# Kernel optimization log

Measured on AMD Instinct MI355X. Metric: run time of the kernel, lower is better.

Reference implementation:

```python
import jax, jax.numpy as jnp
import numpy as np

IN_FEATURES = 896
OUT_FEATURES = 151936  # Qwen2.5 vocab
BATCH, SEQ = 2, 1024


def setup_inputs() -> dict:
    key = jax.random.key(0)
    k1, k2, k3 = jax.random.split(key, 3)
    x = jax.random.normal(k1, (BATCH, SEQ, IN_FEATURES), dtype=jnp.float32)
    # int8-range quantized weights stored as int32 (values in [-127, 127])
    quant_weight = jax.random.randint(k2, (OUT_FEATURES, IN_FEATURES), -127, 128, dtype=jnp.int32)
    # per-output-row scales (positive, small)
    scales = jax.random.uniform(k3, (OUT_FEATURES,), dtype=jnp.float32, minval=0.001, maxval=0.02)
    return {"x": x, "quant_weight": quant_weight, "scales": scales}


def reference(x, quant_weight, scales):
    # dequantize: W = int8_weight * per_row_scale  -> [out, in]
    w = quant_weight.astype(x.dtype) * scales.astype(x.dtype)[:, None]
    # F.linear(x, W, None) == x @ W.T : [b, s, in] x [out, in] -> [b, s, out]
    return jnp.einsum('bsi,oi->bso', x, w)
```

## Files before the change

kernel.cpp:

```cpp
#include <hip/hip_runtime.h>
#include <hip/hip_bf16.h>


#define M_DIM 2048
#define N_DIM 151936
#define K_DIM 896

#define BM 128
#define BN 64
#define BK 64
#define NKT (K_DIM / BK)
#define MB_CNT (M_DIM / BM)
#define NB_CNT (N_DIM / BN)
#define NWG (MB_CNT * NB_CNT)

typedef __attribute__((ext_vector_type(8))) short bf16x8;
typedef __attribute__((ext_vector_type(4))) float f32x4;
typedef __attribute__((ext_vector_type(4))) int   i32x4;
typedef __attribute__((ext_vector_type(4))) unsigned int u32x4;
typedef __attribute__((ext_vector_type(2))) unsigned int u32x2;

static __device__ __forceinline__ unsigned short f2bf(float f) {
    unsigned int u = __builtin_bit_cast(unsigned int, f);
    u += 0x7FFFu + ((u >> 16) & 1u);
    return (unsigned short)(u >> 16);
}
static __device__ __forceinline__ unsigned int pack2(float lo, float hi) {
    return (unsigned int)f2bf(lo) | ((unsigned int)f2bf(hi) << 16);
}
static __device__ __forceinline__ void gload_lds16(const void* g, void* l) {
    __builtin_amdgcn_global_load_lds(
        (const __attribute__((address_space(1))) unsigned int*)g,
        (__attribute__((address_space(3))) unsigned int*)l, 16, 0, 0);
}


__global__ void quant_x_kernel(const float* __restrict__ X,
                               signed char* __restrict__ Xq,
                               float* __restrict__ Sx) {
    const int row  = blockIdx.x * 4 + (threadIdx.x >> 6);
    const int lane = threadIdx.x & 63;
    const float* xr = X + (size_t)row * K_DIM;
    float v[14];
    float am = 0.f;
    #pragma unroll
    for (int i = 0; i < 14; ++i) {
        v[i] = xr[lane + i * 64];
        am = fmaxf(am, fabsf(v[i]));
    }
    #pragma unroll
    for (int off = 32; off > 0; off >>= 1)
        am = fmaxf(am, __shfl_xor(am, off));
    am = fmaxf(am, 1e-20f);
    const float inv = 127.f / am;
    if (lane == 0) Sx[row] = am / 127.f;
    signed char* qr = Xq + (size_t)row * K_DIM;
    #pragma unroll
    for (int i = 0; i < 14; ++i)
        qr[lane + i * 64] = (signed char)(int)rintf(v[i] * inv);
}

__global__ void cvt_w8_kernel(const int* __restrict__ Wq,
                              signed char* __restrict__ W8) {
    const long n8 = (long)N_DIM * K_DIM / 8;
    for (long i = (long)blockIdx.x * blockDim.x + threadIdx.x; i < n8;
         i += (long)gridDim.x * blockDim.x) {
        i32x4 a = ((const i32x4*)Wq)[2 * i];
        i32x4 b = ((const i32x4*)Wq)[2 * i + 1];
        unsigned int lo = (unsigned int)(a[0] & 0xff) |
                          ((unsigned int)(a[1] & 0xff) << 8) |
                          ((unsigned int)(a[2] & 0xff) << 16) |
                          ((unsigned int)(a[3] & 0xff) << 24);
        unsigned int hi = (unsigned int)(b[0] & 0xff) |
                          ((unsigned int)(b[1] & 0xff) << 8) |
                          ((unsigned int)(b[2] & 0xff) << 16) |
                          ((unsigned int)(b[3] & 0xff) << 24);
        u32x2 o; o[0] = lo; o[1] = hi;
        ((u32x2*)W8)[i] = o;
    }
}


#define SCHED0 __builtin_amdgcn_sched_barrier(0)
#define VMCNT0 asm volatile("s_waitcnt vmcnt(0)" ::: "memory")
#define LGKM0  asm volatile("s_waitcnt lgkmcnt(0)" ::: "memory")

__global__ __launch_bounds__(256, 5)
void lmhead_gemm_i8(const signed char* __restrict__ Xq,
                    const signed char* __restrict__ W8,
                    const float* __restrict__ Sw,
                    const float* __restrict__ Sx,
                    float* __restrict__ O)
{
    __shared__ signed char ldsA[2][BM][BK];
    __shared__ signed char ldsB[2][BN][BK];

    const int tid  = threadIdx.x;
    const int lane = tid & 63;
    const int wave = tid >> 6;
    const int wr   = wave >> 1;
    const int wc   = wave & 1;

    const int bid = blockIdx.x;
    const int wg  = (bid & 7) * (NWG / 8) + (bid >> 3);
    const int mb  = wg % MB_CNT;
    const int nb  = wg / MB_CNT;

    const int lslot = (lane & 3) ^ ((lane >> 3) & 3);
    const signed char* srcA =
        Xq + (size_t)(mb * BM + wave * 32 + (lane >> 2)) * K_DIM + lslot * 16;
    const signed char* srcB =
        W8 + (size_t)(nb * BN + wave * 16 + (lane >> 2)) * K_DIM + lslot * 16;

    auto stage = [&](int b2, int k0) {
        gload_lds16(srcA + k0, &ldsA[b2][wave * 32][0]);
        gload_lds16(srcA + (size_t)16 * K_DIM + k0, &ldsA[b2][wave * 32 + 16][0]);
        gload_lds16(srcB + k0, &ldsB[b2][wave * 16][0]);
    };

    const int physoff   = ((lane >> 4) ^ ((lane >> 1) & 3)) * 16;
    const int arow_base = wr * 64 + (lane & 15);
    const int brow_base = wc * 32 + (lane & 15);

    i32x4 acc[4][2];
    #pragma unroll
    for (int i = 0; i < 4; ++i)
        #pragma unroll
        for (int j = 0; j < 2; ++j)
            acc[i][j] = i32x4{0, 0, 0, 0};

    stage(0, 0);
    SCHED0;
    VMCNT0;
    SCHED0;
    __builtin_amdgcn_s_barrier();
    SCHED0;

    i32x4 af[4], bfr[2];

#define READ_AB(B2) do { \
    _Pragma("unroll") \
    for (int mf = 0; mf < 4; ++mf) \
        af[mf] = *(const i32x4*)&ldsA[B2][arow_base + mf * 16][physoff]; \
    _Pragma("unroll") \
    for (int nf = 0; nf < 2; ++nf) \
        bfr[nf] = *(const i32x4*)&ldsB[B2][brow_base + nf * 16][physoff]; \
} while (0)
#define MFMA8() do { \
    __builtin_amdgcn_s_setprio(1); \
    _Pragma("unroll") \
    for (int mf = 0; mf < 4; ++mf) { \
        _Pragma("unroll") \
        for (int nf = 0; nf < 2; ++nf) \
            acc[mf][nf] = __builtin_amdgcn_mfma_i32_16x16x64_i8( \
                af[mf], bfr[nf], acc[mf][nf], 0, 0, 0); \
    } \
    __builtin_amdgcn_s_setprio(0); \
} while (0)

    #pragma unroll 2
    for (int t = 0; t < NKT; ++t) {
        const int cur = t & 1;
        READ_AB(cur);
        if (t < NKT - 1) stage(cur ^ 1, (t + 1) * BK);
        SCHED0;
        VMCNT0;
        LGKM0;
        SCHED0;
        __builtin_amdgcn_s_barrier();
        SCHED0;
        MFMA8();
    }

#undef READ_AB
#undef MFMA8

    __syncthreads();

    float* lf = (float*)&ldsA[0][0][0];
    const int qw = lane >> 4;
    const int li = lane & 15;

    float scn[2];
    #pragma unroll
    for (int nf = 0; nf < 2; ++nf)
        scn[nf] = Sw[nb * BN + wc * 32 + nf * 16 + li];

    #pragma unroll
    for (int p = 0; p < 2; ++p) {
        if (p) __syncthreads();
        if (wr == p) {
            #pragma unroll
            for (int a = 0; a < 4; ++a) {
                #pragma unroll
                for (int nf = 0; nf < 2; ++nf) {
                    #pragma unroll
                    for (int r = 0; r < 4; ++r) {
                        const int lr   = a * 16 + qw * 4 + r;
                        const int col  = wc * 32 + nf * 16 + li;
                        const int pcol = col ^ (qw << 4);
                        lf[lr * 64 + pcol] = (float)acc[a][nf][r] * scn[nf];
                    }
                }
            }
        }
        __syncthreads();
        #pragma unroll
        for (int i = 0; i < 4; ++i) {
            const int row    = i * 16 + (tid >> 4);
            const int lane16 = tid & 15;
            const int q      = (row >> 2) & 3;
            const int pch    = lane16 ^ (q << 2);
            f32x4 v = *(const f32x4*)&lf[row * 64 + pch * 4];
            const size_t grow = (size_t)(mb * BM + p * 64 + row);
            v *= Sx[grow];
            const size_t gcol = (size_t)(nb * BN + lane16 * 4);
            *(f32x4*)&O[grow * N_DIM + gcol] = v;
        }
    }
}


#define FBM 128
#define FBN 128
#define FBK 32
#define FNSTEPS (K_DIM / FBK)
#define FMB (M_DIM / FBM)
#define FNB (N_DIM / FBN)
#define FNWG (FMB * FNB)

__global__ __launch_bounds__(256, 2)
void lmhead_gemm_conv(const float* __restrict__ X,
                      const int* __restrict__ Wq,
                      const float* __restrict__ S,
                      float* __restrict__ O)
{
    __shared__ unsigned short Alds[2][FBM][FBK];
    __shared__ unsigned short Blds2[2][FBN][FBK];

    const int tid  = threadIdx.x;
    const int lane = tid & 63;
    const int wave = tid >> 6;
    const int wr   = wave >> 1;
    const int wc   = wave & 1;

    const int bid = blockIdx.x;
    const int wg  = (bid & 7) * (FNWG / 8) + (bid >> 3);
    const int mb  = wg % FMB;
    const int nb  = wg / FMB;

    const int srow = tid >> 1;
    const int skh  = (tid & 1) * 16;

    const float* aptr = X  + (size_t)(mb * FBM + srow) * K_DIM + skh;
    const int*   wptr = Wq + (size_t)(nb * FBN + srow) * K_DIM + skh;

    f32x4 av[4];
    i32x4 wv[4];

    auto load_tiles = [&](int k0) {
        const f32x4* ap = (const f32x4*)(aptr + k0);
        const i32x4* wp = (const i32x4*)(wptr + k0);
        av[0] = ap[0]; av[1] = ap[1]; av[2] = ap[2]; av[3] = ap[3];
        wv[0] = wp[0]; wv[1] = wp[1]; wv[2] = wp[2]; wv[3] = wp[3];
    };

    auto stage = [&](int buf) {
        unsigned int apk[8], wpk[8];
        #pragma unroll
        for (int i = 0; i < 8; ++i) {
            apk[i] = pack2(av[(2*i) >> 2][(2*i) & 3], av[(2*i+1) >> 2][(2*i+1) & 3]);
            wpk[i] = pack2((float)wv[(2*i) >> 2][(2*i) & 3], (float)wv[(2*i+1) >> 2][(2*i+1) & 3]);
        }
        *(u32x4*)&Alds[buf][srow][skh]      = u32x4{apk[0], apk[1], apk[2], apk[3]};
        *(u32x4*)&Alds[buf][srow][skh + 8]  = u32x4{apk[4], apk[5], apk[6], apk[7]};
        *(u32x4*)&Blds2[buf][srow][skh]     = u32x4{wpk[0], wpk[1], wpk[2], wpk[3]};
        *(u32x4*)&Blds2[buf][srow][skh + 8] = u32x4{wpk[4], wpk[5], wpk[6], wpk[7]};
    };

    f32x4 acc[4][4];
    #pragma unroll
    for (int i = 0; i < 4; ++i)
        #pragma unroll
        for (int j = 0; j < 4; ++j)
            acc[i][j] = f32x4{0.f, 0.f, 0.f, 0.f};

    load_tiles(0);
    stage(0);
    __syncthreads();

    int cur = 0;
    for (int s = 0; s < FNSTEPS; ++s) {
        if (s + 1 < FNSTEPS) load_tiles((s + 1) * FBK);

        bf16x8 af[4], bfr[4];
        const int arow = wr * 64 + (lane & 15);
        const int brow = wc * 64 + (lane & 15);
        const int kb   = (lane >> 4) * 8;
        #pragma unroll
        for (int mf = 0; mf < 4; ++mf)
            af[mf] = *(const bf16x8*)&Alds[cur][arow + mf * 16][kb];
        #pragma unroll
        for (int nf = 0; nf < 4; ++nf)
            bfr[nf] = *(const bf16x8*)&Blds2[cur][brow + nf * 16][kb];

        #pragma unroll
        for (int mf = 0; mf < 4; ++mf)
            #pragma unroll
            for (int nf = 0; nf < 4; ++nf)
                acc[mf][nf] = __builtin_amdgcn_mfma_f32_16x16x32_bf16(
                    af[mf], bfr[nf], acc[mf][nf], 0, 0, 0);

        if (s + 1 < FNSTEPS) stage(cur ^ 1);
        __syncthreads();
        cur ^= 1;
    }

    #pragma unroll
    for (int nf = 0; nf < 4; ++nf) {
        const int n = nb * FBN + wc * 64 + nf * 16 + (lane & 15);
        const float sc = S[n];
        #pragma unroll
        for (int mf = 0; mf < 4; ++mf) {
            const int m0 = mb * FBM + wr * 64 + mf * 16 + ((lane >> 4) << 2);
            #pragma unroll
            for (int r = 0; r < 4; ++r)
                O[(size_t)(m0 + r) * N_DIM + n] = acc[mf][nf][r] * sc;
        }
    }
}


extern "C" void kernel_launch(void* const* d_in, const int* in_sizes, int n_in,
                              void* d_out, int out_size, void* d_ws, size_t ws_size,
                              hipStream_t stream) {
    const float* X  = (const float*)d_in[0];
    const int*   Wq = (const int*)d_in[1];
    const float* S  = (const float*)d_in[2];
    float*       O  = (float*)d_out;

    const size_t XQ_BYTES = (size_t)M_DIM * K_DIM;
    const size_t SX_BYTES = (size_t)M_DIM * sizeof(float);
    const size_t W8_BYTES = (size_t)N_DIM * K_DIM;

    if (ws_size >= XQ_BYTES + SX_BYTES + W8_BYTES) {
        signed char* xq = (signed char*)d_ws;
        float*       sx = (float*)((char*)d_ws + XQ_BYTES);
        signed char* w8 = (signed char*)((char*)d_ws + XQ_BYTES + SX_BYTES);
        quant_x_kernel<<<M_DIM / 4, 256, 0, stream>>>(X, xq, sx);
        cvt_w8_kernel<<<2048, 256, 0, stream>>>(Wq, w8);
        lmhead_gemm_i8<<<NWG, 256, 0, stream>>>(xq, w8, S, sx, O);
    } else {
        lmhead_gemm_conv<<<FNWG, 256, 0, stream>>>(X, Wq, S, O);
    }
}
```

Before: 774.3 us.

## Keep full-K weight strip resident in LDS and stream activations from global

Each workgroup now loads a 128-column by full-K int8 weight strip into LDS once, using about 112 KB. It then loops over 1024 rows of M in chunks of 256, reading A fragments straight from global memory with even/odd register double-buffering. Blocks grow to 512 threads at one block per CU, and the double-buffered per-K-tile LDS staging and per-tile barriers are gone. The epilogue writes scaled results directly from registers instead of staging through LDS. That trades the earlier 16-byte vector stores for scalar stores covering 16 contiguous floats per row, which may hurt write coalescing on this output-heavy kernel.

```diff
diff --git a/kernel.cpp b/kernel.cpp
--- a/kernel.cpp
+++ b/kernel.cpp
@@ -6,13 +6,9 @@
 #define N_DIM 151936
 #define K_DIM 896
 
-#define BM 128
-#define BN 64
-#define BK 64
-#define NKT (K_DIM / BK)
-#define MB_CNT (M_DIM / BM)
-#define NB_CNT (N_DIM / BN)
-#define NWG (MB_CNT * NB_CNT)
+#define NKT 14
+#define NSTRIP (N_DIM / 128)
+#define NWG (NSTRIP * 2)
 
 typedef __attribute__((ext_vector_type(8))) short bf16x8;
 typedef __attribute__((ext_vector_type(4))) float f32x4;
@@ -81,141 +77,120 @@
 }
 
 
-#define SCHED0 __builtin_amdgcn_sched_barrier(0)
-#define VMCNT0 asm volatile("s_waitcnt vmcnt(0)" ::: "memory")
-#define LGKM0  asm volatile("s_waitcnt lgkmcnt(0)" ::: "memory")
-
-__global__ __launch_bounds__(256, 5)
+__global__ __launch_bounds__(512, 1)
 void lmhead_gemm_i8(const signed char* __restrict__ Xq,
                     const signed char* __restrict__ W8,
                     const float* __restrict__ Sw,
                     const float* __restrict__ Sx,
                     float* __restrict__ O)
 {
-    __shared__ signed char ldsA[2][BM][BK];
-    __shared__ signed char ldsB[2][BN][BK];
+    __shared__ signed char Wlds[NKT][128][64];
 
     const int tid  = threadIdx.x;
     const int lane = tid & 63;
     const int wave = tid >> 6;
-    const int wr   = wave >> 1;
+    const int mq   = wave >> 1;
     const int wc   = wave & 1;
 
     const int bid = blockIdx.x;
-    const int wg  = (bid & 7) * (NWG / 8) + (bid >> 3);
-    const int mb  = wg % MB_CNT;
-    const int nb  = wg / MB_CNT;
+    const int xcd = bid & 7, lin = bid >> 3;
+    const int q = NWG / 8, r = NWG % 8;
+    const int wg = (xcd < r ? xcd * (q + 1)
+                            : r * (q + 1) + (xcd - r) * q) + lin;
+    const int nb = wg >> 1;
+    const int mh = wg & 1;
 
     const int lslot = (lane & 3) ^ ((lane >> 3) & 3);
-    const signed char* srcA =
-        Xq + (size_t)(mb * BM + wave * 32 + (lane >> 2)) * K_DIM + lslot * 16;
-    const signed char* srcB =
-        W8 + (size_t)(nb * BN + wave * 16 + (lane >> 2)) * K_DIM + lslot * 16;
-
-    auto stage = [&](int b2, int k0) {
-        gload_lds16(srcA + k0, &ldsA[b2][wave * 32][0]);
-        gload_lds16(srcA + (size_t)16 * K_DIM + k0, &ldsA[b2][wave * 32 + 16][0]);
-        gload_lds16(srcB + k0, &ldsB[b2][wave * 16][0]);
-    };
-
-    const int physoff   = ((lane >> 4) ^ ((lane >> 1) & 3)) * 16;
-    const int arow_base = wr * 64 + (lane & 15);
-    const int brow_base = wc * 32 + (lane & 15);
-
-    i32x4 acc[4][2];
-    #pragma unroll
-    for (int i = 0; i < 4; ++i)
-        #pragma unroll
-        for (int j = 0; j < 2; ++j)
-            acc[i][j] = i32x4{0, 0, 0, 0};
-
-    stage(0, 0);
-    SCHED0;
-    VMCNT0;
-    SCHED0;
-    __builtin_amdgcn_s_barrier();
-    SCHED0;
-
-    i32x4 af[4], bfr[2];
-
-#define READ_AB(B2) do { \
+    const signed char* srcW =
+        W8 + (size_t)(nb * 128 + wave * 16 + (lane >> 2)) * K_DIM + lslot * 16;
+    #pragma unroll
+    for (int kt = 0; kt < NKT; ++kt)
+        gload_lds16(srcW + kt * 64, &Wlds[kt][wave * 16][0]);
+    asm volatile("s_waitcnt vmcnt(0)" ::: "memory");
+    __syncthreads();
+
+    const int physoff = ((lane >> 4) ^ ((lane >> 1) & 3)) * 16;
+    const int brow    = wc * 64 + (lane & 15);
+
+    float scn[4];
+    #pragma unroll
+    for (int nf = 0; nf < 4; ++nf)
+        scn[nf] = Sw[nb * 128 + wc * 64 + nf * 16 + (lane & 15)];
+
+    const int li  = lane & 15;
+    const int qw4 = (lane >> 4) * 4;
+
+    for (int s = 0; s < 4; ++s) {
+        const int mbase = mh * 1024 + s * 256;
+        const int mrow0 = mbase + mq * 64;
+
+        const signed char* aPtr =
+            Xq + (size_t)(mrow0 + li) * K_DIM + (lane >> 4) * 16;
+
+        f32x4 sxv0 = *(const f32x4*)&Sx[mrow0 +  0 + qw4];
+        f32x4 sxv1 = *(const f32x4*)&Sx[mrow0 + 16 + qw4];
+        f32x4 sxv2 = *(const f32x4*)&Sx[mrow0 + 32 + qw4];
+        f32x4 sxv3 = *(const f32x4*)&Sx[mrow0 + 48 + qw4];
+
+        i32x4 acc[4][4];
+        #pragma unroll
+        for (int i = 0; i < 4; ++i)
+            #pragma unroll
+            for (int j = 0; j < 4; ++j)
+                acc[i][j] = i32x4{0, 0, 0, 0};
+
+        i32x4 afE[4], afO[4], bfr[4];
+
+#define LOAD_A(DST, T) do { \
     _Pragma("unroll") \
     for (int mf = 0; mf < 4; ++mf) \
-        af[mf] = *(const i32x4*)&ldsA[B2][arow_base + mf * 16][physoff]; \
+        DST[mf] = *(const i32x4*)(aPtr + (size_t)mf * 16 * K_DIM + (T) * 64); \
+} while (0)
+#define READ_B(T) do { \
     _Pragma("unroll") \
-    for (int nf = 0; nf < 2; ++nf) \
-        bfr[nf] = *(const i32x4*)&ldsB[B2][brow_base + nf * 16][physoff]; \
+    for (int nf = 0; nf < 4; ++nf) \
+        bfr[nf] = *(const i32x4*)&Wlds[T][brow + nf * 16][physoff]; \
 } while (0)
-#define MFMA8() do { \
-    __builtin_amdgcn_s_setprio(1); \
+#define MFMA16(AF) do { \
     _Pragma("unroll") \
     for (int mf = 0; mf < 4; ++mf) { \
         _Pragma("unroll") \
-        for (int nf = 0; nf < 2; ++nf) \
+        for (int nf = 0; nf < 4; ++nf) \
             acc[mf][nf] = __builtin_amdgcn_mfma_i32_16x16x64_i8( \
-                af[mf], bfr[nf], acc[mf][nf], 0, 0, 0); \
+                AF[mf], bfr[nf], acc[mf][nf], 0, 0, 0); \
     } \
-    __builtin_amdgcn_s_setprio(0); \
 } while (0)
 
-    #pragma unroll 2
-    for (int t = 0; t < NKT; ++t) {
-        const int cur = t & 1;
-        READ_AB(cur);
-        if (t < NKT - 1) stage(cur ^ 1, (t + 1) * BK);
-        SCHED0;
-        VMCNT0;
-        LGKM0;
-        SCHED0;
-        __builtin_amdgcn_s_barrier();
-        SCHED0;
-        MFMA8();
-    }
-
-#undef READ_AB
-#undef MFMA8
-
-    __syncthreads();
-
-    float* lf = (float*)&ldsA[0][0][0];
-    const int qw = lane >> 4;
-    const int li = lane & 15;
-
-    float scn[2];
-    #pragma unroll
-    for (int nf = 0; nf < 2; ++nf)
-        scn[nf] = Sw[nb * BN + wc * 32 + nf * 16 + li];
-
-    #pragma unroll
-    for (int p = 0; p < 2; ++p) {
-        if (p) __syncthreads();
-        if (wr == p) {
+        LOAD_A(afE, 0);
+        #pragma unroll
+        for (int tt = 0; tt < NKT; tt += 2) {
+            if (tt + 1 < NKT) LOAD_A(afO, tt + 1);
+            READ_B(tt);
+            MFMA16(afE);
+            if (tt + 2 < NKT) LOAD_A(afE, tt + 2);
+            READ_B(tt + 1);
+            MFMA16(afO);
+        }
+
+#undef LOAD_A
+#undef READ_B
+#undef MFMA16
+
+        #pragma unroll
+        for (int mf = 0; mf < 4; ++mf) {
+            const f32x4 sxv = (mf == 0) ? sxv0 : (mf == 1) ? sxv1
+                            : (mf == 2) ? sxv2 : sxv3;
             #pragma unroll
-            for (int a = 0; a < 4; ++a) {
+            for (int nf = 0; nf < 4; ++nf) {
+                const float sc = scn[nf];
+                const size_t gcol = (size_t)(nb * 128 + wc * 64 + nf * 16 + li);
                 #pragma unroll
-                for (int nf = 0; nf < 2; ++nf) {
-                    #pragma unroll
-                    for (int r = 0; r < 4; ++r) {
-                        const int lr   = a * 16 + qw * 4 + r;
-                        const int col  = wc * 32 + nf * 16 + li;
-                        const int pcol = col ^ (qw << 4);
-                        lf[lr * 64 + pcol] = (float)acc[a][nf][r] * scn[nf];
-                    }
+                for (int rr = 0; rr < 4; ++rr) {
+                    const size_t grow = (size_t)(mrow0 + mf * 16 + qw4 + rr);
+                    O[grow * N_DIM + gcol] =
+                        (float)acc[mf][nf][rr] * sc * sxv[rr];
                 }
             }
-        }
-        __syncthreads();
-        #pragma unroll
-        for (int i = 0; i < 4; ++i) {
-            const int row    = i * 16 + (tid >> 4);
-            const int lane16 = tid & 15;
-            const int q      = (row >> 2) & 3;
-            const int pch    = lane16 ^ (q << 2);
-            f32x4 v = *(const f32x4*)&lf[row * 64 + pch * 4];
-            const size_t grow = (size_t)(mb * BM + p * 64 + row);
-            v *= Sx[grow];
-            const size_t gcol = (size_t)(nb * BN + lane16 * 4);
-            *(f32x4*)&O[grow * N_DIM + gcol] = v;
         }
     }
 }
@@ -349,7 +324,7 @@
         signed char* w8 = (signed char*)((char*)d_ws + XQ_BYTES + SX_BYTES);
         quant_x_kernel<<<M_DIM / 4, 256, 0, stream>>>(X, xq, sx);
         cvt_w8_kernel<<<2048, 256, 0, stream>>>(Wq, w8);
-        lmhead_gemm_i8<<<NWG, 256, 0, stream>>>(xq, w8, S, sx, O);
+        lmhead_gemm_i8<<<NWG, 512, 0, stream>>>(xq, w8, S, sx, O);
     } else {
         lmhead_gemm_conv<<<FNWG, 256, 0, stream>>>(X, Wq, S, O);
     }
```

Result: slower. 1.250 ms (+61.4%).
